# Performance work log

Measured on AMD Instinct MI355X. Metric: run time of the kernel, lower is better.

The kernel has to match this reference:

```python
import jax, jax.numpy as jnp
import numpy as np

N = 100000          # nodes
E = 2000000         # edges
NUM_ET = 10         # num_edge_types
ED = 16             # edge_embedding_dim
LAYERS = [(64, 4, 16), (64, 4, 8)]  # (in_channels, heads, out_channels_per_head)
NEG_SLOPE = 0.2     # PyG GATConv default leaky_relu slope


def setup_inputs() -> dict:
    key = jax.random.key(0)
    ks = jax.random.split(key, 4 + 6 * len(LAYERS))
    inp = {
        "x": jax.random.normal(ks[0], (N, LAYERS[0][0]), jnp.float32),
        "edge_index": jax.random.randint(ks[1], (2, E), 0, N),
        "edge_type": jax.random.randint(ks[2], (E,), 0, NUM_ET),
        "edge_emb": jax.random.normal(ks[3], (NUM_ET, ED), jnp.float32) * 0.1,
    }
    k = 4
    for i, (cin, H, C) in enumerate(LAYERS):
        s = 1.0 / np.sqrt(cin)
        inp[f"l{i}_lin_w"] = jax.random.normal(ks[k], (H * C, cin), jnp.float32) * s; k += 1
        inp[f"l{i}_att_src"] = jax.random.normal(ks[k], (H, C), jnp.float32) * 0.1; k += 1
        inp[f"l{i}_att_dst"] = jax.random.normal(ks[k], (H, C), jnp.float32) * 0.1; k += 1
        inp[f"l{i}_lin_e_w"] = jax.random.normal(ks[k], (H * C, ED), jnp.float32) * (1.0 / np.sqrt(ED)); k += 1
        inp[f"l{i}_att_e"] = jax.random.normal(ks[k], (H, C), jnp.float32) * 0.1; k += 1
        inp[f"l{i}_bias"] = jnp.zeros((H * C,), jnp.float32); k += 1
    return inp


def gat_conv(x, src, dst, edge_attr, lin_w, a_src, a_dst, lin_e_w, a_e, bias, H, C):
    n = x.shape[0]
    h = (x @ lin_w.T).reshape(n, H, C)                 # [N,H,C]
    e = (edge_attr @ lin_e_w.T).reshape(-1, H, C)      # [E',H,C]
    s_src = jnp.einsum('nhc,hc->nh', h, a_src)
    s_dst = jnp.einsum('nhc,hc->nh', h, a_dst)
    alpha = s_src[src] + s_dst[dst] + jnp.einsum('ehc,hc->eh', e, a_e)  # [E',H]
    alpha = jax.nn.leaky_relu(alpha, NEG_SLOPE)
    # segment softmax over edges grouped by destination node
    amax = jax.ops.segment_max(alpha, dst, num_segments=n)
    ex = jnp.exp(alpha - amax[dst])
    denom = jax.ops.segment_sum(ex, dst, num_segments=n)
    w = ex / denom[dst]                                # [E',H]
    out = jax.ops.segment_sum(h[src] * w[..., None], dst, num_segments=n)
    return out.reshape(n, H * C) + bias


def reference(x, edge_index, edge_type, edge_emb,
              l0_lin_w, l0_att_src, l0_att_dst, l0_lin_e_w, l0_att_e, l0_bias,
              l1_lin_w, l1_att_src, l1_att_dst, l1_lin_e_w, l1_att_e, l1_bias):
    n = x.shape[0]
    edge_attr = edge_emb[edge_type]                    # [E,ED]
    # PyG GATConv default: add self-loops, fill their edge_attr with the mean
    loop = jnp.arange(n)
    src = jnp.concatenate([edge_index[0], loop])
    dst = jnp.concatenate([edge_index[1], loop])
    mean_attr = jnp.mean(edge_attr, axis=0)
    ea = jnp.concatenate([edge_attr, jnp.broadcast_to(mean_attr, (n, ED))], axis=0)

    h = gat_conv(x, src, dst, ea, l0_lin_w, l0_att_src, l0_att_dst,
                 l0_lin_e_w, l0_att_e, l0_bias, LAYERS[0][1], LAYERS[0][2])
    h = jax.nn.relu(h)  # dropout disabled (eval mode)
    out = gat_conv(h, src, dst, ea, l1_lin_w, l1_att_src, l1_att_dst,
                   l1_lin_e_w, l1_att_e, l1_bias, LAYERS[1][1], LAYERS[1][2])
    return out
```

## Files before the change

### kernel.cpp

```cpp
#include <hip/hip_runtime.h>
#include <hip/hip_fp16.h>
#include <cstdint>
#include <type_traits>

#define LRELU(a) ((a) > 0.f ? (a) : 0.2f * (a))
#define BBITS 9
#define BSZ   (1 << BBITS)
#define MAXB  256
#define SL    8
#define PSTR  12288
#define SLOT  48
#define SLOT4 (SLOT / 4)
#define LIDX(e) (((((e) >> 21) & (BSZ - 1)) * SL) + ((((e) & 131071)) >> 14))
#define PKCAP 3072

typedef float cfloat4 __attribute__((ext_vector_type(4)));

__global__ __launch_bounds__(1024) void k13_scatter(
        const int* __restrict__ ei, const int* __restrict__ ety, int E,
        int* __restrict__ staging, int* __restrict__ bcnt, int* __restrict__ tcnt,
        int BSTRIDE) {
    __shared__ int ent[4096], ent2[4096];
    __shared__ unsigned char ebb[4096], ebb2[4096];
    __shared__ int lh[MAXB], lstart[MAXB], lcur[MAXB], sc[MAXB];
    __shared__ int lt[16];
    int t = threadIdx.x;
    if (t < 256) lh[t] = 0;
    if (t < 16) lt[t] = 0;
    __syncthreads();
    int base = blockIdx.x * 4096;
    int cnt = min(4096, E - base);
    for (int i = t; i < cnt; i += 1024) {
        int s = ei[base + i], d = ei[E + base + i], ty = ety[base + i];
        int b = d >> BBITS;
        ent[i] = s | (ty << 17) | ((d & (BSZ - 1)) << 21);
        ebb[i] = (unsigned char)b;
        atomicAdd(&lh[b], 1);
        atomicAdd(&lt[ty], 1);
    }
    __syncthreads();
    if (t < 256) sc[t] = lh[t];
    __syncthreads();
    for (int off = 1; off < 256; off <<= 1) {
        int a = (t >= off && t < 256) ? sc[t - off] : 0;
        __syncthreads();
        if (t < 256) sc[t] += a;
        __syncthreads();
    }
    if (t < 256) { lstart[t] = sc[t] - lh[t]; lcur[t] = lstart[t]; }
    __syncthreads();
    for (int i = t; i < cnt; i += 1024) {
        int b = ebb[i];
        int pos = atomicAdd(&lcur[b], 1);
        ent2[pos] = ent[i];
        ebb2[pos] = (unsigned char)b;
    }
    __syncthreads();
    for (int i = t; i < cnt; i += 1024) {
        int b = ebb2[i];
        int p = i - lstart[b];
        if (p < SLOT) staging[(size_t)b * BSTRIDE + blockIdx.x * SLOT + p] = ent2[i];
    }
    if (t < 256) bcnt[blockIdx.x * 256 + t] = lh[t];
    if (t < 16)  tcnt[blockIdx.x * 16 + t]  = lt[t];
}

template <int OUT, int C, typename XT>
__device__ void gemm_role(char* ldsbuf, int bid, const XT* __restrict__ x,
                          const float* __restrict__ W,
                          const float* __restrict__ asrc, const float* __restrict__ adst,
                          int N, __half* __restrict__ hout,
                          float* __restrict__ ssrc, float* __restrict__ sdst) {
    const int JG = OUT / 4;
    const int RG = 256 / JG;
    const int RPT = 64 / RG;
    const int WTP = OUT + 4;
    const int WQ = WTP / 4;
    float* xs = (float*)ldsbuf;
    cfloat4* wt4 = (cfloat4*)(ldsbuf + 64 * 68 * 4);
    float* wt = (float*)wt4;
    int t = threadIdx.x;
    for (int idx = t; idx < OUT * 64; idx += 256) {
        int j = idx >> 6, k = idx & 63;
        wt[k * WTP + j] = W[idx];
    }
    int rowbase = bid * 64;
    int nrows = min(64, N - rowbase);
    if constexpr (std::is_same<XT, float>::value) {
        const float4* px = (const float4*)x;
        for (int idx = t; idx < nrows * 16; idx += 256) {
            int r = idx >> 4, kq = idx & 15;
            float4 v = px[(size_t)(rowbase + r) * 16 + kq];
            float* dst = xs + r * 68 + kq * 4;
            dst[0] = v.x; dst[1] = v.y; dst[2] = v.z; dst[3] = v.w;
        }
    } else {
        const uint4* px = (const uint4*)x;
        for (int idx = t; idx < nrows * 8; idx += 256) {
            int r = idx >> 3, ko = idx & 7;
            uint4 u = px[(size_t)(rowbase + r) * 8 + ko];
            const __half2* hp = (const __half2*)&u;
            float* dst = xs + r * 68 + ko * 8;
#pragma unroll
            for (int i = 0; i < 4; ++i) {
                float2 f = __half22float2(hp[i]);
                dst[2 * i] = f.x;
                dst[2 * i + 1] = f.y;
            }
        }
    }
    if (nrows < 64)
        for (int idx = nrows * 64 + t; idx < 64 * 64; idx += 256)
            xs[(idx >> 6) * 68 + (idx & 63)] = 0.f;
    __syncthreads();
    int jg = t % JG, rg = t / JG;
    cfloat4 acc[RPT];
#pragma unroll
    for (int rr = 0; rr < RPT; ++rr) acc[rr] = cfloat4{0.f, 0.f, 0.f, 0.f};
    const float* xrow = xs + rg * RPT * 68;
#pragma unroll 4
    for (int k = 0; k < 64; ++k) {
        cfloat4 wv = wt4[k * WQ + jg];
#pragma unroll
        for (int rr = 0; rr < RPT; ++rr) acc[rr] += xrow[rr * 68 + k] * wv;
    }
    const int JH = C / 4;
    cfloat4 avs = ((const cfloat4*)asrc)[jg];
    cfloat4 avd = ((const cfloat4*)adst)[jg];
    int hd = jg / JH;
#pragma unroll
    for (int rr = 0; rr < RPT; ++rr) {
        int r = rg * RPT + rr;
        int row = rowbase + r;
        bool ok = r < nrows;
        if (ok) {
            ushort4 pk;
            pk.x = __half_as_ushort(__float2half(acc[rr][0]));
            pk.y = __half_as_ushort(__float2half(acc[rr][1]));
            pk.z = __half_as_ushort(__float2half(acc[rr][2]));
            pk.w = __half_as_ushort(__float2half(acc[rr][3]));
            *(ushort4*)(hout + (size_t)row * OUT + jg * 4) = pk;
        }
        float ps = acc[rr][0] * avs[0] + acc[rr][1] * avs[1] + acc[rr][2] * avs[2] + acc[rr][3] * avs[3];
        float pd = acc[rr][0] * avd[0] + acc[rr][1] * avd[1] + acc[rr][2] * avd[2] + acc[rr][3] * avd[3];
#pragma unroll
        for (int w = 1; w < JH; w <<= 1) {
            ps += __shfl_xor(ps, w);
            pd += __shfl_xor(pd, w);
        }
        if ((jg & (JH - 1)) == 0 && ok) {
            ssrc[row * 4 + hd] = ps;
            sdst[row * 4 + hd] = pd;
        }
    }
}

__device__ void k4_role(char* ldsbuf, int b, const int* __restrict__ staging,
                        const int* __restrict__ bcnt, int egrid, int BSTRIDE,
                        int N, int2* __restrict__ rowptr2, int* __restrict__ packed) {
    int* lcnt = (int*)ldsbuf;
    int* lcur = lcnt + BSZ * SL;
    int* tsum = lcur + BSZ * SL;
    int* cnts = tsum + 256;
    int t = threadIdx.x;
    int n0 = b << BBITS;
    for (int i = t; i < BSZ * SL; i += 256) lcnt[i] = 0;
    for (int k = t; k < 512; k += 256) cnts[k] = (k < egrid) ? min(bcnt[k * 256 + b], SLOT) : 0;
    __syncthreads();
    const int4* st4 = (const int4*)(staging + (size_t)b * BSTRIDE);
    int tot4 = egrid * SLOT4;
    for (int i = t; i < tot4; i += 256) {
        int k = i / SLOT4;
        int j0 = (i - k * SLOT4) * 4;
        int c = cnts[k];
        if (j0 < c) {
            int4 e4 = st4[i];
            int nv = c - j0;
            atomicAdd(&lcnt[LIDX(e4.x)], 1);
            if (nv > 1) atomicAdd(&lcnt[LIDX(e4.y)], 1);
            if (nv > 2) atomicAdd(&lcnt[LIDX(e4.z)], 1);
            if (nv > 3) atomicAdd(&lcnt[LIDX(e4.w)], 1);
        }
    }
    __syncthreads();
    int loc[2 * SL];
    int run = 0;
#pragma unroll
    for (int n = 0; n < 2; ++n)
#pragma unroll
        for (int j = 0; j < SL; ++j) {
            loc[n * SL + j] = run;
            run += lcnt[(2 * t + n) * SL + j];
        }
    tsum[t] = run;
    __syncthreads();
    for (int off = 1; off < 256; off <<= 1) {
        int a = (t >= off) ? tsum[t - off] : 0;
        __syncthreads();
        tsum[t] += a;
        __syncthreads();
    }
    int nbase = tsum[t] - run;
    int run0 = loc[SL];
    int node = n0 + 2 * t;
    int pbase = b * PSTR;
    if (node < N)     rowptr2[node]     = make_int2(pbase + nbase, pbase + nbase + run0);
    if (node + 1 < N) rowptr2[node + 1] = make_int2(pbase + nbase + run0, pbase + nbase + run);
#pragma unroll
    for (int n = 0; n < 2; ++n)
#pragma unroll
        for (int j = 0; j < SL; ++j) lcur[(2 * t + n) * SL + j] = nbase + loc[n * SL + j];
    __syncthreads();
    for (int i = t; i < tot4; i += 256) {
        int k = i / SLOT4;
        int j0 = (i - k * SLOT4) * 4;
        int c = cnts[k];
        if (j0 < c) {
            int4 e4 = st4[i];
            int nv = c - j0;
            int pos = atomicAdd(&lcur[LIDX(e4.x)], 1);
            if (pos < PSTR) packed[pbase + pos] = e4.x & 0x1FFFFF;
            if (nv > 1) {
                pos = atomicAdd(&lcur[LIDX(e4.y)], 1);
                if (pos < PSTR) packed[pbase + pos] = e4.y & 0x1FFFFF;
            }
            if (nv > 2) {
                pos = atomicAdd(&lcur[LIDX(e4.z)], 1);
                if (pos < PSTR) packed[pbase + pos] = e4.z & 0x1FFFFF;
            }
            if (nv > 3) {
                pos = atomicAdd(&lcur[LIDX(e4.w)], 1);
                if (pos < PSTR) packed[pbase + pos] = e4.w & 0x1FFFFF;
            }
        }
    }
}

__device__ void finalize_role(char* ldsbuf, const int* __restrict__ tcnt, int egrid, int E,
                              const float* __restrict__ emb,
                              const float* __restrict__ we0, const float* __restrict__ ae0,
                              const float* __restrict__ we1, const float* __restrict__ ae1,
                              float* __restrict__ alphaE) {
    int* part = (int*)ldsbuf;
    int* tot  = part + 256;
    float* tmp = (float*)(tot + 16);
    int t = threadIdx.x;
    int ty = t & 15, chunk = t >> 4;
    int s = 0;
    for (int k = chunk; k < egrid; k += 16) s += tcnt[k * 16 + ty];
    part[t] = s;
    __syncthreads();
    if (t < 16) {
        int v = 0;
        for (int p = 0; p < 16; ++p) v += part[p * 16 + t];
        tot[t] = v;
    }
    __syncthreads();
    if (t < 80) {
        int l = t / 40, r = t % 40, ty2 = r >> 2, h = r & 3;
        const float* w = l ? we1 : we0;
        const float* ae = l ? ae1 : ae0;
        int CC = l ? 8 : 16;
        const float* ev = emb + ty2 * 16;
        float val = 0.f;
        for (int c = 0; c < CC; ++c) {
            const float* wr = w + (h * CC + c) * 16;
            float s2 = 0.f;
            for (int d = 0; d < 16; ++d) s2 += wr[d] * ev[d];
            val += s2 * ae[h * CC + c];
        }
        tmp[l * 44 + ty2 * 4 + h] = val;
        alphaE[l * 44 + ty2 * 4 + h] = val;
    }
    __syncthreads();
    if (t < 8) {
        int l = t >> 2, h = t & 3;
        float s3 = 0.f;
        for (int ty3 = 0; ty3 < 10; ++ty3)
            s3 += (float)tot[ty3] * tmp[l * 44 + ty3 * 4 + h];
        alphaE[l * 44 + 40 + h] = s3 / (float)E;
    }
}

__global__ __launch_bounds__(256) void fused_gemm0_k4(
        int nK4, int nGemm,
        const float* __restrict__ x, const float* __restrict__ W,
        const float* __restrict__ asrc, const float* __restrict__ adst, int N,
        __half* __restrict__ hout, float* __restrict__ ssrc, float* __restrict__ sdst,
        const int* __restrict__ staging, const int* __restrict__ bcnt,
        int egrid, int BSTRIDE, int2* __restrict__ rowptr2, int* __restrict__ packed,
        const int* __restrict__ tcnt, int E,
        const float* __restrict__ emb,
        const float* __restrict__ we0, const float* __restrict__ ae0,
        const float* __restrict__ we1, const float* __restrict__ ae1,
        float* __restrict__ alphaE) {
    __shared__ __align__(16) char lds[35840];
    if (blockIdx.x < (unsigned)nK4)
        k4_role(lds, blockIdx.x, staging, bcnt, egrid, BSTRIDE, N, rowptr2, packed);
    else if (blockIdx.x < (unsigned)(nK4 + nGemm))
        gemm_role<64, 16, float>(lds, blockIdx.x - nK4, x, W, asrc, adst, N,
                                 hout, ssrc, sdst);
    else
        finalize_role(lds, tcnt, egrid, E, emb, we0, ae0, we1, ae1, alphaE);
}

__global__ __launch_bounds__(256) void gemmscore1(const __half* __restrict__ x,
                                                  const float* __restrict__ W,
                                                  const float* __restrict__ asrc,
                                                  const float* __restrict__ adst, int N,
                                                  __half* __restrict__ hout,
                                                  float* __restrict__ ssrc,
                                                  float* __restrict__ sdst) {
    __shared__ __align__(16) char lds[64 * 68 * 4 + 64 * 9 * 16];
    gemm_role<32, 8, __half>(lds, blockIdx.x, x, W, asrc, adst, N, hout, ssrc, sdst);
}

__device__ inline void fma_h8(float* acc, float4 v, float ex) {
    const __half2* h2 = (const __half2*)&v;
#pragma unroll
    for (int i = 0; i < 4; ++i) {
        float2 f = __half22float2(h2[i]);
        acc[2 * i]     += ex * f.x;
        acc[2 * i + 1] += ex * f.y;
    }
}

template <int C, int TPN, bool RELU, typename OT>
__global__ __launch_bounds__(256) void agg_kernel(const int2* __restrict__ rp2,
                                                  const int* __restrict__ packed,
                                                  const __half* __restrict__ hmat,
                                                  const float* __restrict__ ssrc,
                                                  const float* __restrict__ sdst,
                                                  const float* __restrict__ alphaE,
                                                  const float* __restrict__ bias, int N,
                                                  OT* __restrict__ out) {
    const int HALVES = TPN / 4;
    const int CPT = 4 * C / TPN;
    const int VEC = CPT / 8;
    const int NPB = 256 / TPN;
    __shared__ float aE[44];
    __shared__ int pk_lds[PKCAP];
    __shared__ int sspan;
    int t = threadIdx.x;
    if (t < 44) aE[t] = alphaE[t];
    int nfirst = blockIdx.x * NPB;
    if (nfirst >= N) return;
    int nlast = min(nfirst + NPB, N) - 1;
    if (t == 0) sspan = rp2[nlast].y - rp2[nfirst].x;
    __syncthreads();
    int beg0 = rp2[nfirst].x;
    int span = sspan;
    bool uselds = span <= PKCAP;
    if (uselds)
        for (int i = t; i < span; i += 256) pk_lds[i] = packed[beg0 + i];
    __syncthreads();
    int g = nfirst + t / TPN;
    if (g >= N) return;
    int node = g;
    int sub  = t % TPN;
    int hd   = sub / HALVES;
    int off  = hd * C + (sub % HALVES) * CPT;
    const int ROW = 4 * C;
    int2 be = rp2[node];
    int beg = be.x, end = be.y;
    int deg = end - beg;
    const int* pkp = uselds ? (const int*)(pk_lds + (beg - beg0)) : (packed + beg);
    float sd = sdst[node * 4 + hd];
    float m = LRELU(ssrc[node * 4 + hd] + sd + aE[40 + hd]);
    float denom = 1.f;
    float acc[CPT];
#pragma unroll
    for (int c = 0; c < CPT; ++c) acc[c] = 0.f;
#pragma unroll
    for (int v = 0; v < VEC; ++v) {
        float4 sv = *(const float4*)(hmat + (size_t)node * ROW + off + 8 * v);
        fma_h8(acc + 8 * v, sv, 1.f);
    }
    int k = 0;
    for (; k + 4 <= deg; k += 4) {
        int p0 = pkp[k], p1 = pkp[k + 1], p2 = pkp[k + 2], p3 = pkp[k + 3];
        int n0 = p0 & 131071, n1 = p1 & 131071, n2 = p2 & 131071, n3 = p3 & 131071;
        float v0 = ssrc[n0 * 4 + hd], v1 = ssrc[n1 * 4 + hd];
        float v2 = ssrc[n2 * 4 + hd], v3 = ssrc[n3 * 4 + hd];
        float4 r0[VEC], r1[VEC], r2[VEC], r3[VEC];
#pragma unroll
        for (int v = 0; v < VEC; ++v) {
            r0[v] = *(const float4*)(hmat + (size_t)n0 * ROW + off + 8 * v);
            r1[v] = *(const float4*)(hmat + (size_t)n1 * ROW + off + 8 * v);
            r2[v] = *(const float4*)(hmat + (size_t)n2 * ROW + off + 8 * v);
            r3[v] = *(const float4*)(hmat + (size_t)n3 * ROW + off + 8 * v);
        }
        float a0 = LRELU(v0 + sd + aE[((p0 >> 17) & 15) * 4 + hd]);
        float a1 = LRELU(v1 + sd + aE[((p1 >> 17) & 15) * 4 + hd]);
        float a2 = LRELU(v2 + sd + aE[((p2 >> 17) & 15) * 4 + hd]);
        float a3 = LRELU(v3 + sd + aE[((p3 >> 17) & 15) * 4 + hd]);
        float mn = fmaxf(fmaxf(a0, a1), fmaxf(a2, a3));
        if (mn > m) {
            float r = __expf(m - mn);
            denom *= r;
#pragma unroll
            for (int c = 0; c < CPT; ++c) acc[c] *= r;
            m = mn;
        }
        float e0 = __expf(a0 - m), e1 = __expf(a1 - m);
        float e2 = __expf(a2 - m), e3 = __expf(a3 - m);
        denom += (e0 + e1) + (e2 + e3);
#pragma unroll
        for (int v = 0; v < VEC; ++v) {
            fma_h8(acc + 8 * v, r0[v], e0);
            fma_h8(acc + 8 * v, r1[v], e1);
            fma_h8(acc + 8 * v, r2[v], e2);
            fma_h8(acc + 8 * v, r3[v], e3);
        }
    }
    for (; k < deg; ++k) {
        int p0 = pkp[k];
        int n0 = p0 & 131071;
        float v0 = ssrc[n0 * 4 + hd];
        float4 r0[VEC];
#pragma unroll
        for (int v = 0; v < VEC; ++v)
            r0[v] = *(const float4*)(hmat + (size_t)n0 * ROW + off + 8 * v);
        float a0 = LRELU(v0 + sd + aE[((p0 >> 17) & 15) * 4 + hd]);
        if (a0 > m) {
            float r = __expf(m - a0);
            denom *= r;
#pragma unroll
            for (int c = 0; c < CPT; ++c) acc[c] *= r;
            m = a0;
        }
        float e0 = __expf(a0 - m);
        denom += e0;
#pragma unroll
        for (int v = 0; v < VEC; ++v) fma_h8(acc + 8 * v, r0[v], e0);
    }
    float inv = 1.f / denom;
    if constexpr (std::is_same<OT, __half>::value) {
#pragma unroll
        for (int v = 0; v < VEC; ++v) {
            union { cfloat4 vv; __half h[8]; } u;
#pragma unroll
            for (int c = 0; c < 8; ++c) {
                float a = fmaf(acc[8 * v + c], inv, bias[off + 8 * v + c]);
                if (RELU) a = fmaxf(a, 0.f);
                u.h[c] = __float2half(a);
            }
            cfloat4* op = (cfloat4*)(out + (size_t)node * ROW + off + 8 * v);
            __builtin_nontemporal_store(u.vv, op);
        }
    } else {
#pragma unroll
        for (int v = 0; v < VEC; ++v) {
            cfloat4 o0, o1;
#pragma unroll
            for (int c = 0; c < 4; ++c) {
                float a = fmaf(acc[8 * v + c], inv, bias[off + 8 * v + c]);
                float bq = fmaf(acc[8 * v + c + 4], inv, bias[off + 8 * v + c + 4]);
                if (RELU) { a = fmaxf(a, 0.f); bq = fmaxf(bq, 0.f); }
                o0[c] = a;
                o1[c] = bq;
            }
            cfloat4* op = (cfloat4*)(out + (size_t)node * ROW + off + 8 * v);
            __builtin_nontemporal_store(o0, op);
            __builtin_nontemporal_store(o1, op + 1);
        }
    }
}

extern "C" void kernel_launch(void* const* d_in, const int* in_sizes, int n_in,
                              void* d_out, int out_size, void* d_ws, size_t ws_size,
                              hipStream_t stream) {
    const float* x    = (const float*)d_in[0];
    const int*   ei   = (const int*)d_in[1];
    const int*   ety  = (const int*)d_in[2];
    const float* emb  = (const float*)d_in[3];
    const float* w0   = (const float*)d_in[4];
    const float* as0  = (const float*)d_in[5];
    const float* ad0  = (const float*)d_in[6];
    const float* we0  = (const float*)d_in[7];
    const float* ae0  = (const float*)d_in[8];
    const float* b0   = (const float*)d_in[9];
    const float* w1   = (const float*)d_in[10];
    const float* as1  = (const float*)d_in[11];
    const float* ad1  = (const float*)d_in[12];
    const float* we1  = (const float*)d_in[13];
    const float* ae1  = (const float*)d_in[14];
    const float* b1   = (const float*)d_in[15];

    const int N = in_sizes[0] / 64;
    const int E = in_sizes[1] / 2;
    const int NB = (N + BSZ - 1) >> BBITS;
    const int egrid = (E + 4095) / 4096;
    const int BSTRIDE = egrid * SLOT;

    char* ws = (char*)d_ws;
    size_t o = 0;
    auto alloc = [&](size_t bytes) { size_t r = o; o = (o + bytes + 255) & ~(size_t)255; return r; };
    size_t o_alphaE   = alloc(4 * 88);
    size_t o_bcnt     = alloc((size_t)4 * egrid * 256);
    size_t o_tcnt     = alloc((size_t)4 * egrid * 16);
    size_t o_rowptr2  = alloc((size_t)8 * N);
    size_t o_staging  = alloc((size_t)4 * NB * BSTRIDE);
    size_t o_packed   = alloc((size_t)4 * NB * PSTR);
    size_t o_h        = alloc((size_t)2 * N * 64);
    size_t o_x1h      = alloc((size_t)2 * N * 64);
    size_t o_ssrc     = alloc((size_t)4 * N * 4);
    size_t o_sdst     = alloc((size_t)4 * N * 4);
    (void)ws_size;

    float*  alphaE   = (float*)(ws + o_alphaE);
    int*    bcnt     = (int*)(ws + o_bcnt);
    int*    tcnt     = (int*)(ws + o_tcnt);
    int2*   rowptr2  = (int2*)(ws + o_rowptr2);
    int*    staging  = (int*)(ws + o_staging);
    int*    packed   = (int*)(ws + o_packed);
    __half* h0       = (__half*)(ws + o_h);
    __half* x1h      = (__half*)(ws + o_x1h);
    float*  ssrc     = (float*)(ws + o_ssrc);
    float*  sdst     = (float*)(ws + o_sdst);
    float*  outp     = (float*)d_out;

    int ggrid = (N + 63) / 64;

    k13_scatter<<<egrid, 1024, 0, stream>>>(ei, ety, E, staging, bcnt, tcnt, BSTRIDE);
    fused_gemm0_k4<<<NB + ggrid + 1, 256, 0, stream>>>(
        NB, ggrid, x, w0, as0, ad0, N, h0, ssrc, sdst,
        staging, bcnt, egrid, BSTRIDE, rowptr2, packed,
        tcnt, E, emb, we0, ae0, we1, ae1, alphaE);

    int agg_grid = (N * 4 + 255) / 256;

    agg_kernel<16, 4, true, __half><<<agg_grid, 256, 0, stream>>>(rowptr2, packed, h0,
                                                                  ssrc, sdst, alphaE,
                                                                  b0, N, x1h);
    gemmscore1<<<ggrid, 256, 0, stream>>>(x1h, w1, as1, ad1, N, h0, ssrc, sdst);
    agg_kernel<8, 4, false, float><<<agg_grid, 256, 0, stream>>>(rowptr2, packed, h0,
                                                                 ssrc, sdst, alphaE + 44,
                                                                 b1, N, outp);
}
```

Before: 242.7 us.

## Fuse layer-1 linear projection and attention scores into layer-0 aggregation epilogue

Removes the separate gemmscore1 kernel. The layer-0 aggregation now applies bias and ReLU, then multiplies the 64-wide row by the layer-1 weights held in shared memory, using shuffles across the 4 threads of each node. It writes the fp16 h1 rows and the layer-1 source and destination scores directly. This avoids writing and re-reading the intermediate x1 activations and one kernel launch, at the cost of more registers and an 8 KB weight staging copy per block in the aggregation kernel.

```diff
diff --git a/kernel.cpp b/kernel.cpp
--- a/kernel.cpp
+++ b/kernel.cpp
@@ -304,17 +304,6 @@
         finalize_role(lds, tcnt, egrid, E, emb, we0, ae0, we1, ae1, alphaE);
 }
 
-__global__ __launch_bounds__(256) void gemmscore1(const __half* __restrict__ x,
-                                                  const float* __restrict__ W,
-                                                  const float* __restrict__ asrc,
-                                                  const float* __restrict__ adst, int N,
-                                                  __half* __restrict__ hout,
-                                                  float* __restrict__ ssrc,
-                                                  float* __restrict__ sdst) {
-    __shared__ __align__(16) char lds[64 * 68 * 4 + 64 * 9 * 16];
-    gemm_role<32, 8, __half>(lds, blockIdx.x, x, W, asrc, adst, N, hout, ssrc, sdst);
-}
-
 __device__ inline void fma_h8(float* acc, float4 v, float ex) {
     const __half2* h2 = (const __half2*)&v;
 #pragma unroll
@@ -325,7 +314,7 @@
     }
 }
 
-template <int C, int TPN, bool RELU, typename OT>
+template <int C, int TPN, bool RELU, bool FUSE1, typename OT>
 __global__ __launch_bounds__(256) void agg_kernel(const int2* __restrict__ rp2,
                                                   const int* __restrict__ packed,
                                                   const __half* __restrict__ hmat,
@@ -333,7 +322,12 @@
                                                   const float* __restrict__ sdst,
                                                   const float* __restrict__ alphaE,
                                                   const float* __restrict__ bias, int N,
-                                                  OT* __restrict__ out) {
+                                                  OT* __restrict__ out,
+                                                  const float* __restrict__ w1,
+                                                  const float* __restrict__ as1,
+                                                  const float* __restrict__ ad1,
+                                                  float* __restrict__ ssrc1,
+                                                  float* __restrict__ sdst1) {
     const int HALVES = TPN / 4;
     const int CPT = 4 * C / TPN;
     const int VEC = CPT / 8;
@@ -341,12 +335,18 @@
     __shared__ float aE[44];
     __shared__ int pk_lds[PKCAP];
     __shared__ int sspan;
+    __shared__ float w1s[FUSE1 ? 2048 : 1];
+    __shared__ float as1s[FUSE1 ? 32 : 1], ad1s[FUSE1 ? 32 : 1];
     int t = threadIdx.x;
     if (t < 44) aE[t] = alphaE[t];
     int nfirst = blockIdx.x * NPB;
     if (nfirst >= N) return;
     int nlast = min(nfirst + NPB, N) - 1;
     if (t == 0) sspan = rp2[nlast].y - rp2[nfirst].x;
+    if constexpr (FUSE1) {
+        for (int i = t; i < 2048; i += 256) w1s[i] = w1[i];
+        if (t < 32) { as1s[t] = as1[t]; ad1s[t] = ad1[t]; }
+    }
     __syncthreads();
     int beg0 = rp2[nfirst].x;
     int span = sspan;
@@ -435,7 +435,43 @@
         for (int v = 0; v < VEC; ++v) fma_h8(acc + 8 * v, r0[v], e0);
     }
     float inv = 1.f / denom;
-    if constexpr (std::is_same<OT, __half>::value) {
+    if constexpr (FUSE1) {
+        float x1v[16];
+#pragma unroll
+        for (int c = 0; c < 16; ++c)
+            x1v[c] = fmaxf(fmaf(acc[c], inv, bias[off + c]), 0.f);
+        float ps = 0.f, pd = 0.f;
+        __half h8[8];
+#pragma unroll
+        for (int jj = 0; jj < 4; ++jj) {
+            float hv[8];
+#pragma unroll
+            for (int jo = 0; jo < 8; ++jo) {
+                const float* wr = w1s + (jj * 8 + jo) * 64 + sub * 16;
+                float p = 0.f;
+#pragma unroll
+                for (int c = 0; c < 16; ++c) p = fmaf(x1v[c], wr[c], p);
+                hv[jo] = p;
+            }
+#pragma unroll
+            for (int jo = 0; jo < 8; ++jo) {
+                hv[jo] += __shfl_xor(hv[jo], 1);
+                hv[jo] += __shfl_xor(hv[jo], 2);
+            }
+            if (jj == sub) {
+#pragma unroll
+                for (int jo = 0; jo < 8; ++jo) {
+                    ps = fmaf(hv[jo], as1s[jj * 8 + jo], ps);
+                    pd = fmaf(hv[jo], ad1s[jj * 8 + jo], pd);
+                    h8[jo] = __float2half(hv[jo]);
+                }
+            }
+        }
+        __builtin_nontemporal_store(*(const cfloat4*)h8,
+                                    (cfloat4*)((__half*)out + (size_t)node * 32 + sub * 8));
+        ssrc1[node * 4 + sub] = ps;
+        sdst1[node * 4 + sub] = pd;
+    } else if constexpr (std::is_same<OT, __half>::value) {
 #pragma unroll
         for (int v = 0; v < VEC; ++v) {
             union { cfloat4 vv; __half h[8]; } u;
@@ -506,6 +542,8 @@
     size_t o_x1h      = alloc((size_t)2 * N * 64);
     size_t o_ssrc     = alloc((size_t)4 * N * 4);
     size_t o_sdst     = alloc((size_t)4 * N * 4);
+    size_t o_ssrc1    = alloc((size_t)4 * N * 4);
+    size_t o_sdst1    = alloc((size_t)4 * N * 4);
     (void)ws_size;
 
     float*  alphaE   = (float*)(ws + o_alphaE);
@@ -515,9 +553,11 @@
     int*    staging  = (int*)(ws + o_staging);
     int*    packed   = (int*)(ws + o_packed);
     __half* h0       = (__half*)(ws + o_h);
-    __half* x1h      = (__half*)(ws + o_x1h);
+    __half* h1       = (__half*)(ws + o_x1h);
     float*  ssrc     = (float*)(ws + o_ssrc);
     float*  sdst     = (float*)(ws + o_sdst);
+    float*  ssrc1    = (float*)(ws + o_ssrc1);
+    float*  sdst1    = (float*)(ws + o_sdst1);
     float*  outp     = (float*)d_out;
 
     int ggrid = (N + 63) / 64;
@@ -530,11 +570,10 @@
 
     int agg_grid = (N * 4 + 255) / 256;
 
-    agg_kernel<16, 4, true, __half><<<agg_grid, 256, 0, stream>>>(rowptr2, packed, h0,
-                                                                  ssrc, sdst, alphaE,
-                                                                  b0, N, x1h);
-    gemmscore1<<<ggrid, 256, 0, stream>>>(x1h, w1, as1, ad1, N, h0, ssrc, sdst);
-    agg_kernel<8, 4, false, float><<<agg_grid, 256, 0, stream>>>(rowptr2, packed, h0,
-                                                                 ssrc, sdst, alphaE + 44,
-                                                                 b1, N, outp);
-}
+    agg_kernel<16, 4, true, true, __half><<<agg_grid, 256, 0, stream>>>(
+        rowptr2, packed, h0, ssrc, sdst, alphaE, b0, N, h1,
+        w1, as1, ad1, ssrc1, sdst1);
+    agg_kernel<8, 4, false, false, float><<<agg_grid, 256, 0, stream>>>(
+        rowptr2, packed, h1, ssrc1, sdst1, alphaE + 44, b1, N, outp,
+        nullptr, nullptr, nullptr, nullptr, nullptr);
+}
```

Measured after the change: 234.9 us, median of 2. -3.2%, faster.
